# Performance work log

Measured on AMD Instinct MI355X. Metric: run time of the kernel, lower is better.

The kernel has to match this reference:

```python
import jax, jax.numpy as jnp
import numpy as np

B, L, D_IN, D_MODEL, D_STATE, D_DISCR, KER = 2, 1024, 512, 1024, 16, 64, 4


def setup_inputs() -> dict:
    ks = jax.random.split(jax.random.key(0), 9)
    s = 0.02
    return {
        "seq": jax.random.normal(ks[0], (B, L, D_IN), jnp.float32),
        "W_in": jax.random.normal(ks[1], (2 * D_MODEL, D_IN), jnp.float32) * s,
        "W_out": jax.random.normal(ks[2], (D_IN, D_MODEL), jnp.float32) * s,
        "W_B": jax.random.normal(ks[3], (D_STATE, D_MODEL), jnp.float32) * s,
        "W_C": jax.random.normal(ks[4], (D_STATE, D_MODEL), jnp.float32) * s,
        "W_D1": jax.random.normal(ks[5], (D_DISCR, D_MODEL), jnp.float32) * s,
        "W_D2": jax.random.normal(ks[6], (D_MODEL, D_DISCR), jnp.float32) * s,
        "conv_w": jax.random.normal(ks[7], (D_MODEL, 1, KER), jnp.float32) * 0.1,
        "conv_b": jax.random.normal(ks[8], (D_MODEL,), jnp.float32) * 0.01,
        "A": jnp.tile(jnp.arange(1, D_STATE + 1, dtype=jnp.float32), (D_MODEL, 1)),
        "D": jnp.ones((D_MODEL,), jnp.float32),
    }


def _causal_depthwise_conv(x, w, b):
    # x: [B, L, D] -> torch Conv1d(groups=D, padding=KER-1) truncated to first L outputs
    x = jnp.swapaxes(x, 1, 2)  # [B, D, L]
    y = jax.lax.conv_general_dilated(
        x, w, window_strides=(1,), padding=[(KER - 1, 0)],
        dimension_numbers=("NCH", "OIH", "NCH"), feature_group_count=D_MODEL)
    y = y + b[None, :, None]
    return jnp.swapaxes(y, 1, 2)  # [B, L, D]


def _ssm(x, W_B, W_C, W_D1, W_D2, A, D):
    # x: [B, L, D]
    exp_negA = jnp.exp(-A)                                  # [D, S]
    Bm = jnp.einsum("bld,sd->bls", x, W_B)                  # [B, L, S]
    Cm = jnp.einsum("bld,sd->bls", x, W_C)                  # [B, L, S]
    delta = jax.nn.softplus(D + jnp.einsum("ble,de->bld", jnp.einsum("bld,ed->ble", x, W_D1), W_D2))  # [B, L, D]
    A_bar = exp_negA[None, None] * delta[..., None]         # [B, L, D, S]
    X = Bm[:, :, None, :] * delta[..., None] * x[..., None]  # [B, L, D, S]

    def comb(c1, c2):
        a1, x1 = c1
        a2, x2 = c2
        return a1 * a2, a2 * x1 + x2

    _, h = jax.lax.associative_scan(comb, (A_bar, X), axis=1)  # h: [B, L, D, S]
    y = jnp.einsum("blds,bls->bld", h, Cm)
    return y + D * x


def reference(seq, W_in, W_out, W_B, W_C, W_D1, W_D2, conv_w, conv_b, A, D):
    ab = jnp.einsum("bli,oi->blo", seq, W_in)   # [B, L, 2*D_MODEL]
    a, b = ab[..., :D_MODEL], ab[..., D_MODEL:]
    a = jax.nn.silu(_causal_depthwise_conv(a, conv_w, conv_b))
    a = _ssm(a, W_B, W_C, W_D1, W_D2, A, D)
    out = a * jax.nn.silu(b)
    return jnp.einsum("bld,od->blo", out, W_out)  # [B, L, D_IN]
```

## Files before the change

kernel.cpp:

```cpp
#include <hip/hip_runtime.h>
#include <hip/hip_bf16.h>

using bf16 = __hip_bfloat16;
typedef short short8 __attribute__((ext_vector_type(8)));
typedef float float4v __attribute__((ext_vector_type(4)));

#define B_   2
#define L_   1024
#define DIN  512
#define DM   1024
#define DS   16
#define DD   64
#define KER_ 4
#define NROW (B_*L_)

#define SD   8
#define SC   32
#define SLC  32
#define SDP  9

__device__ __forceinline__ float silu_f(float v){ return v / (1.f + expf(-v)); }

__device__ __forceinline__ short2 f2bf2(float a, float b) {
  __hip_bfloat162 h = __float22bfloat162_rn(float2{a, b});
  union { __hip_bfloat162 h; short2 s; } u; u.h = h; return u.s;
}

template<int MW, int NW, int MT, int NT, int EP, int KS, int B3SRC, int CONVA>
__global__ __launch_bounds__(256)
void mfma_nt(const float* __restrict__ A, const float* __restrict__ B,
             const float* __restrict__ B2, const float* __restrict__ B3,
             float* __restrict__ C, const float* __restrict__ Dv,
             const float* __restrict__ abp, const float* __restrict__ cw,
             const float* __restrict__ cb,
             int M, int N, int K, int lda, int ldb, int ldc) {
  constexpr int BM = MW * MT * 16;
  constexpr int BN = NW * NT * 16;
  constexpr int TU = (BM + BN) * 4;
  constexpr int NU = (TU + 255) / 256;
  __shared__ short As[BM * 40];
  __shared__ short Bs[BN * 40];
  const int m0 = blockIdx.y * BM;
  const int n0 = blockIdx.x * BN;
  const int tid  = threadIdx.x;
  const int lane = tid & 63;
  const int wave = tid >> 6;
  const int wm   = wave % MW;
  const int wn   = wave / MW;
  const int r16  = lane & 15;
  const int quad = lane >> 4;
  const int kb   = (KS > 1) ? blockIdx.z : 0;
  const int kper = K / KS;
  const int kbeg = kb * kper;
  const int kend = kbeg + kper;

  float4v acc[MT][NT];
#pragma unroll
  for (int i = 0; i < MT; i++)
#pragma unroll
    for (int j = 0; j < NT; j++) acc[i][j] = (float4v){0.f, 0.f, 0.f, 0.f};

  float4 pf0[NU], pf1[NU];
  auto ldu = [&](int j, int k0) {
    int u = tid + j * 256;
    if (u >= TU) return;
    if (CONVA && u < BM * 4) {
      int row = u >> 2, q = u & 3;
      int n = m0 + row, l = n & (L_ - 1), bq = n >> 10;
      float4 tap0[KER_], tap1[KER_];
#pragma unroll
      for (int t = 0; t < KER_; t++) {
        int ll = l - (KER_ - 1) + t;
        if (ll >= 0) {
          const float4* p = (const float4*)(abp + (size_t)(bq * L_ + ll) * lda + k0 + q * 8);
          tap0[t] = p[0]; tap1[t] = p[1];
        } else {
          tap0[t] = float4{0.f,0.f,0.f,0.f}; tap1[t] = float4{0.f,0.f,0.f,0.f};
        }
      }
      float r[8];
#pragma unroll
      for (int e = 0; e < 8; e++) {
        int d = k0 + q * 8 + e;
        float4 w = *(const float4*)(cw + d * 4);
        float a = cb[d];
#pragma unroll
        for (int t = 0; t < KER_; t++) {
          float te = (e < 4) ? (&tap0[t].x)[e] : (&tap1[t].x)[e - 4];
          a += te * (&w.x)[t];
        }
        r[e] = silu_f(a);
      }
      pf0[j] = float4{r[0], r[1], r[2], r[3]};
      pf1[j] = float4{r[4], r[5], r[6], r[7]};
      return;
    }
    const float4* p;
    if (u < BM * 4) {
      int row = u >> 2, q = u & 3;
      p = (const float4*)(A + (size_t)(m0 + row) * lda + k0 + q * 8);
    } else {
      int v = u - BM * 4; int row = v >> 2, q = v & 3;
      if (B3SRC) {
        int rr = n0 + row;
        const float* bp = (rr < 16) ? (B + (size_t)rr * ldb)
                        : (rr < 32) ? (B2 + (size_t)(rr - 16) * ldb)
                                    : (B3 + (size_t)(rr - 32) * ldb);
        p = (const float4*)(bp + k0 + q * 8);
      } else {
        p = (const float4*)(B + (size_t)(n0 + row) * ldb + k0 + q * 8);
      }
    }
    pf0[j] = p[0]; pf1[j] = p[1];
  };
  auto stu = [&](int j) {
    int u = tid + j * 256;
    if (u >= TU) return;
    short2 s0 = f2bf2(pf0[j].x, pf0[j].y), s1 = f2bf2(pf0[j].z, pf0[j].w);
    short2 s2 = f2bf2(pf1[j].x, pf1[j].y), s3 = f2bf2(pf1[j].z, pf1[j].w);
    short8 s = { s0.x, s0.y, s1.x, s1.y, s2.x, s2.y, s3.x, s3.y };
    if (u < BM * 4) {
      int row = u >> 2, q = u & 3;
      *(short8*)&As[row * 40 + q * 8] = s;
    } else {
      int v = u - BM * 4; int row = v >> 2, q = v & 3;
      *(short8*)&Bs[row * 40 + q * 8] = s;
    }
  };

#pragma unroll
  for (int j = 0; j < NU; j++) ldu(j, kbeg);

  for (int k0 = kbeg; k0 < kend; k0 += 32) {
#pragma unroll
    for (int j = 0; j < NU; j++) stu(j);
    __syncthreads();
    if (k0 + 32 < kend) {
#pragma unroll
      for (int j = 0; j < NU; j++) ldu(j, k0 + 32);
    }
    short8 afr[MT], bfr[NT];
#pragma unroll
    for (int mi = 0; mi < MT; mi++)
      afr[mi] = *(const short8*)&As[(wm * MT * 16 + mi * 16 + r16) * 40 + quad * 8];
#pragma unroll
    for (int ni = 0; ni < NT; ni++)
      bfr[ni] = *(const short8*)&Bs[(wn * NT * 16 + ni * 16 + r16) * 40 + quad * 8];
#pragma unroll
    for (int mi = 0; mi < MT; mi++)
#pragma unroll
      for (int ni = 0; ni < NT; ni++)
        acc[mi][ni] = __builtin_amdgcn_mfma_f32_16x16x32_bf16(
            afr[mi], bfr[ni], acc[mi][ni], 0, 0, 0);
    __syncthreads();
  }

  float* Cp = C + ((EP == 2) ? (size_t)0 : (size_t)kb * M * ldc);
#pragma unroll
  for (int mi = 0; mi < MT; mi++)
#pragma unroll
    for (int ni = 0; ni < NT; ni++) {
      int gn = n0 + wn * NT * 16 + ni * 16 + r16;
#pragma unroll
      for (int r = 0; r < 4; r++) {
        int gm = m0 + wm * MT * 16 + mi * 16 + quad * 4 + r;
        float v = acc[mi][ni][r];
        if (EP == 1) {
          v += Dv[gn];
          v = fmaxf(v, 0.f) + log1pf(expf(-fabsf(v)));
          Cp[(size_t)gm * ldc + gn] = v;
        } else if (EP == 2) {
          atomicAdd(&Cp[(size_t)gm * ldc + gn], v);
        } else {
          Cp[(size_t)gm * ldc + gn] = v;
        }
      }
    }
}

__global__ __launch_bounds__(256)
void scan_fused_k(const float* __restrict__ ab, const float* __restrict__ dlt,
                  const float* __restrict__ pall, const float* __restrict__ A,
                  const float* __restrict__ Dv, const float* __restrict__ cw,
                  const float* __restrict__ cb, float* __restrict__ sout) {
  __shared__ float Pl[SC][DS][SDP];
  __shared__ float Hl[SC][DS][SDP];
  const int blk = blockIdx.x;
  const int b   = blk >> 7;
  const int d0  = (blk & 127) * SD;
  const int dd  = threadIdx.x & (SD - 1);
  const int c   = threadIdx.x >> 3;
  const int d   = d0 + dd;

  float e[DS];
#pragma unroll
  for (int s = 0; s < DS; s++) e[s] = expf(-A[d * DS + s]);
  const int   lbase = c * SLC;
  const int   nbase = b * L_ + lbase;
  const float4 w    = *(const float4*)(cw + d * 4);
  const float  cbv  = cb[d];

  auto abA = [&](int l) -> float {
    return (l >= 0) ? ab[(size_t)(b * L_ + l) * (2 * DM) + d] : 0.f;
  };

  float r0 = abA(lbase - 3), r1 = abA(lbase - 2), r2 = abA(lbase - 1);
  float h[DS], p[DS];
#pragma unroll
  for (int s = 0; s < DS; s++) { h[s] = 0.f; p[s] = 1.f; }
  for (int i = 0; i < SLC; i++) {
    int n = nbase + i;
    float a3 = ab[(size_t)n * (2 * DM) + d];
    float xv = silu_f(cbv + r0 * w.x + r1 * w.y + r2 * w.z + a3 * w.w);
    r0 = r1; r1 = r2; r2 = a3;
    float dl = dlt[(size_t)n * DM + d];
    float dx = dl * xv;
    const float4* bm4 = (const float4*)(pall + (size_t)n * 96);
    float4 b0 = bm4[0], b1 = bm4[1], b2 = bm4[2], b3 = bm4[3];
    float bmv[DS] = { b0.x,b0.y,b0.z,b0.w, b1.x,b1.y,b1.z,b1.w,
                      b2.x,b2.y,b2.z,b2.w, b3.x,b3.y,b3.z,b3.w };
#pragma unroll
    for (int s = 0; s < DS; s++) {
      float a_ = e[s] * dl;
      h[s] = a_ * h[s] + bmv[s] * dx;
      p[s] *= a_;
    }
  }
#pragma unroll
  for (int s = 0; s < DS; s++) { Pl[c][s][dd] = p[s]; Hl[c][s][dd] = h[s]; }
  __syncthreads();

  if (threadIdx.x < DS * SD) {
    int s2  = threadIdx.x >> 3;
    int dd2 = threadIdx.x & (SD - 1);
    float H = 0.f;
    for (int c2 = 0; c2 < SC; c2++) {
      float pp = Pl[c2][s2][dd2];
      float hh = Hl[c2][s2][dd2];
      Pl[c2][s2][dd2] = H;
      H = pp * H + hh;
    }
  }
  __syncthreads();

#pragma unroll
  for (int s = 0; s < DS; s++) h[s] = Pl[c][s][dd];
  float Dd = Dv[d];
  r0 = abA(lbase - 3); r1 = abA(lbase - 2); r2 = abA(lbase - 1);
  for (int i = 0; i < SLC; i++) {
    int n = nbase + i;
    float a3 = ab[(size_t)n * (2 * DM) + d];
    float xv = silu_f(cbv + r0 * w.x + r1 * w.y + r2 * w.z + a3 * w.w);
    r0 = r1; r1 = r2; r2 = a3;
    float dl = dlt[(size_t)n * DM + d];
    float dx = dl * xv;
    const float4* bm4 = (const float4*)(pall + (size_t)n * 96);
    float4 b0 = bm4[0], b1 = bm4[1], b2 = bm4[2], b3 = bm4[3];
    float4 c0 = bm4[4], c1 = bm4[5], c2v = bm4[6], c3 = bm4[7];
    float bmv[DS] = { b0.x,b0.y,b0.z,b0.w, b1.x,b1.y,b1.z,b1.w,
                      b2.x,b2.y,b2.z,b2.w, b3.x,b3.y,b3.z,b3.w };
    float cmv[DS] = { c0.x,c0.y,c0.z,c0.w, c1.x,c1.y,c1.z,c1.w,
                      c2v.x,c2v.y,c2v.z,c2v.w, c3.x,c3.y,c3.z,c3.w };
    float y = 0.f;
#pragma unroll
    for (int s = 0; s < DS; s++) {
      h[s] = e[s] * dl * h[s] + bmv[s] * dx;
      y += h[s] * cmv[s];
    }
    y += Dd * xv;
    float g = ab[(size_t)n * (2 * DM) + DM + d];
    sout[(size_t)n * DM + d] = y * silu_f(g);
  }
}

extern "C" void kernel_launch(void* const* d_in, const int* in_sizes, int n_in,
                              void* d_out, int out_size, void* d_ws, size_t ws_size,
                              hipStream_t stream) {
  const float* seq  = (const float*)d_in[0];
  const float* Win  = (const float*)d_in[1];
  const float* Wout = (const float*)d_in[2];
  const float* WB   = (const float*)d_in[3];
  const float* WC   = (const float*)d_in[4];
  const float* WD1  = (const float*)d_in[5];
  const float* WD2  = (const float*)d_in[6];
  const float* cw   = (const float*)d_in[7];
  const float* cb   = (const float*)d_in[8];
  const float* A    = (const float*)d_in[9];
  const float* Dv   = (const float*)d_in[10];
  float* out = (float*)d_out;

  float* ws   = (float*)d_ws;
  float* ab   = ws;
  float* dlt  = ab   + 4194304;
  float* pall = dlt  + 2097152;
  float* sout = pall + 196608;
  float* t1   = pall + 32;

  hipMemsetAsync(out, 0, (size_t)NROW * DIN * 4, stream);
  hipMemsetAsync(pall, 0, (size_t)NROW * 96 * 4, stream);
  mfma_nt<2, 2, 4, 2, 0, 1, 0, 0><<<dim3((2 * DM) / 64, NROW / 128, 1), 256, 0, stream>>>(
      seq, Win, nullptr, nullptr, ab, nullptr, nullptr, nullptr, nullptr,
      NROW, 2 * DM, DIN, DIN, DIN, 2 * DM);
  mfma_nt<4, 1, 1, 6, 2, 8, 1, 1><<<dim3(1, NROW / 64, 8), 256, 0, stream>>>(
      nullptr, WB, WC, WD1, pall, nullptr, ab, cw, cb,
      NROW, 96, DM, 2 * DM, DM, 96);
  mfma_nt<2, 2, 2, 2, 1, 1, 0, 0><<<dim3(DM / 64, NROW / 64, 1), 256, 0, stream>>>(
      t1, WD2, nullptr, nullptr, dlt, Dv, nullptr, nullptr, nullptr,
      NROW, DM, DD, 96, DD, DM);
  scan_fused_k<<<B_ * (DM / SD), 256, 0, stream>>>(ab, dlt, pall, A, Dv, cw, cb, sout);
  mfma_nt<2, 2, 2, 2, 2, 2, 0, 0><<<dim3(DIN / 64, NROW / 64, 2), 256, 0, stream>>>(
      sout, Wout, nullptr, nullptr, out, nullptr, nullptr, nullptr, nullptr,
      NROW, DIN, DM, DM, DM, DIN);
}
```

Baseline: 180.4 us.

## Fuse all stages into one persistent kernel with grid barriers

Replaces five kernel launches and two memsets with a single persistent 256-block kernel that runs the input GEMM, the B/C/delta projection, the chunked scan and the output GEMM as phases separated by atomic grid barriers. The delta projection is fused into the projection phase through a shared-memory t1 tile, and split-K atomics are dropped so the memsets go away. The aim is to cut launch gaps and memset overhead, at the cost of fixed tiling per phase, idle blocks in the projection phase (only 128 of 256 work), half the threads idle during the scan, and a reliance on all 256 blocks being co-resident for the barriers.

```diff
diff --git a/kernel.cpp b/kernel.cpp
--- a/kernel.cpp
+++ b/kernel.cpp
@@ -1,7 +1,6 @@
 #include <hip/hip_runtime.h>
 #include <hip/hip_bf16.h>
 
-using bf16 = __hip_bfloat16;
 typedef short short8 __attribute__((ext_vector_type(8)));
 typedef float float4v __attribute__((ext_vector_type(4)));
 
@@ -13,6 +12,8 @@
 #define DD   64
 #define KER_ 4
 #define NROW (B_*L_)
+#define NBLK 256
+#define NTHR 512
 
 #define SD   8
 #define SC   32
@@ -25,251 +26,322 @@
   __hip_bfloat162 h = __float22bfloat162_rn(float2{a, b});
   union { __hip_bfloat162 h; short2 s; } u; u.h = h; return u.s;
 }
-
-template<int MW, int NW, int MT, int NT, int EP, int KS, int B3SRC, int CONVA>
-__global__ __launch_bounds__(256)
-void mfma_nt(const float* __restrict__ A, const float* __restrict__ B,
-             const float* __restrict__ B2, const float* __restrict__ B3,
-             float* __restrict__ C, const float* __restrict__ Dv,
-             const float* __restrict__ abp, const float* __restrict__ cw,
-             const float* __restrict__ cb,
-             int M, int N, int K, int lda, int ldb, int ldc) {
-  constexpr int BM = MW * MT * 16;
-  constexpr int BN = NW * NT * 16;
-  constexpr int TU = (BM + BN) * 4;
-  constexpr int NU = (TU + 255) / 256;
-  __shared__ short As[BM * 40];
-  __shared__ short Bs[BN * 40];
-  const int m0 = blockIdx.y * BM;
-  const int n0 = blockIdx.x * BN;
+__device__ __forceinline__ short f2bf1(float a) {
+  __hip_bfloat16 h = __float2bfloat16(a);
+  union { __hip_bfloat16 h; short s; } u; u.h = h; return u.s;
+}
+__device__ __forceinline__ short8 pack8(const float4& x0, const float4& x1) {
+  short2 s0 = f2bf2(x0.x, x0.y), s1 = f2bf2(x0.z, x0.w);
+  short2 s2 = f2bf2(x1.x, x1.y), s3 = f2bf2(x1.z, x1.w);
+  return short8{ s0.x, s0.y, s1.x, s1.y, s2.x, s2.y, s3.x, s3.y };
+}
+
+union SMem {
+  struct { short As[128 * 40]; short Bs[128 * 40]; } g1;
+  struct { short xs[16 * 40]; short wsb[96 * 40]; short t1s[16 * 72]; } pj;
+  struct { float Pl[SC][DS][SDP]; float Hl[SC][DS][SDP]; } sc;
+  struct { short As[64 * 40]; short Bs[64 * 40]; } g2;
+};
+
+__device__ __forceinline__ void grid_barrier(unsigned* cnt, unsigned nblk) {
+  __syncthreads();
+  if (threadIdx.x == 0) {
+    __threadfence();
+    __hip_atomic_fetch_add(cnt, 1u, __ATOMIC_ACQ_REL, __HIP_MEMORY_SCOPE_AGENT);
+    while (__hip_atomic_load(cnt, __ATOMIC_ACQUIRE, __HIP_MEMORY_SCOPE_AGENT) < nblk)
+      __builtin_amdgcn_s_sleep(1);
+  }
+  __syncthreads();
+  __threadfence();
+}
+
+__global__ __launch_bounds__(NTHR)
+void mega_k(const float* __restrict__ seq, const float* __restrict__ Win,
+            const float* __restrict__ Wout, const float* __restrict__ WB,
+            const float* __restrict__ WC, const float* __restrict__ WD1,
+            const float* __restrict__ WD2, const float* __restrict__ cw,
+            const float* __restrict__ cb, const float* __restrict__ Aa,
+            const float* __restrict__ Dv, float* __restrict__ out,
+            float* __restrict__ ab, float* __restrict__ dlt,
+            float* __restrict__ pall, float* __restrict__ sout,
+            unsigned* __restrict__ bar) {
+  __shared__ SMem sm;
+  const int blk  = blockIdx.x;
   const int tid  = threadIdx.x;
   const int lane = tid & 63;
   const int wave = tid >> 6;
-  const int wm   = wave % MW;
-  const int wn   = wave / MW;
   const int r16  = lane & 15;
   const int quad = lane >> 4;
-  const int kb   = (KS > 1) ? blockIdx.z : 0;
-  const int kper = K / KS;
-  const int kbeg = kb * kper;
-  const int kend = kbeg + kper;
-
-  float4v acc[MT][NT];
-#pragma unroll
-  for (int i = 0; i < MT; i++)
-#pragma unroll
-    for (int j = 0; j < NT; j++) acc[i][j] = (float4v){0.f, 0.f, 0.f, 0.f};
-
-  float4 pf0[NU], pf1[NU];
-  auto ldu = [&](int j, int k0) {
-    int u = tid + j * 256;
-    if (u >= TU) return;
-    if (CONVA && u < BM * 4) {
-      int row = u >> 2, q = u & 3;
-      int n = m0 + row, l = n & (L_ - 1), bq = n >> 10;
-      float4 tap0[KER_], tap1[KER_];
-#pragma unroll
-      for (int t = 0; t < KER_; t++) {
-        int ll = l - (KER_ - 1) + t;
-        if (ll >= 0) {
-          const float4* p = (const float4*)(abp + (size_t)(bq * L_ + ll) * lda + k0 + q * 8);
-          tap0[t] = p[0]; tap1[t] = p[1];
-        } else {
-          tap0[t] = float4{0.f,0.f,0.f,0.f}; tap1[t] = float4{0.f,0.f,0.f,0.f};
+
+  {
+    const int m0 = (blk >> 4) * 128;
+    const int n0 = (blk & 15) * 128;
+    const int wm = wave & 1, wn = wave >> 1;
+    float4v acc[4][2];
+#pragma unroll
+    for (int i = 0; i < 4; i++)
+#pragma unroll
+      for (int j = 0; j < 2; j++) acc[i][j] = (float4v){0.f, 0.f, 0.f, 0.f};
+    float4 pf0[2], pf1[2];
+    auto ldu = [&](int j, int k0) {
+      int u = tid + j * 512;
+      const float4* p;
+      if (u < 512) { int row = u >> 2, q = u & 3;
+        p = (const float4*)(seq + (size_t)(m0 + row) * DIN + k0 + q * 8);
+      } else { int v = u - 512; int row = v >> 2, q = v & 3;
+        p = (const float4*)(Win + (size_t)(n0 + row) * DIN + k0 + q * 8);
+      }
+      pf0[j] = p[0]; pf1[j] = p[1];
+    };
+    auto stu = [&](int j) {
+      int u = tid + j * 512;
+      short8 s = pack8(pf0[j], pf1[j]);
+      if (u < 512) { int row = u >> 2, q = u & 3; *(short8*)&sm.g1.As[row * 40 + q * 8] = s; }
+      else { int v = u - 512; int row = v >> 2, q = v & 3; *(short8*)&sm.g1.Bs[row * 40 + q * 8] = s; }
+    };
+    ldu(0, 0); ldu(1, 0);
+    for (int k0 = 0; k0 < DIN; k0 += 32) {
+      stu(0); stu(1);
+      __syncthreads();
+      if (k0 + 32 < DIN) { ldu(0, k0 + 32); ldu(1, k0 + 32); }
+      short8 afr[4], bfr[2];
+#pragma unroll
+      for (int mi = 0; mi < 4; mi++)
+        afr[mi] = *(const short8*)&sm.g1.As[(wm * 64 + mi * 16 + r16) * 40 + quad * 8];
+#pragma unroll
+      for (int ni = 0; ni < 2; ni++)
+        bfr[ni] = *(const short8*)&sm.g1.Bs[(wn * 32 + ni * 16 + r16) * 40 + quad * 8];
+#pragma unroll
+      for (int mi = 0; mi < 4; mi++)
+#pragma unroll
+        for (int ni = 0; ni < 2; ni++)
+          acc[mi][ni] = __builtin_amdgcn_mfma_f32_16x16x32_bf16(afr[mi], bfr[ni], acc[mi][ni], 0, 0, 0);
+      __syncthreads();
+    }
+#pragma unroll
+    for (int mi = 0; mi < 4; mi++)
+#pragma unroll
+      for (int ni = 0; ni < 2; ni++)
+#pragma unroll
+        for (int r = 0; r < 4; r++)
+          ab[(size_t)(m0 + wm * 64 + mi * 16 + quad * 4 + r) * (2 * DM)
+             + n0 + wn * 32 + ni * 16 + r16] = acc[mi][ni][r];
+  }
+  grid_barrier(bar + 0, NBLK);
+
+  if (blk < 128) {
+    const int m0 = blk * 16;
+    const int bq = m0 >> 10;
+    float4v accp = (float4v){0.f, 0.f, 0.f, 0.f};
+    for (int k0 = 0; k0 < DM; k0 += 32) {
+      if (tid < 64) {
+        int row = tid >> 2, q = tid & 3;
+        int n = m0 + row, l = n & (L_ - 1);
+        float4 tap0[KER_], tap1[KER_];
+#pragma unroll
+        for (int t = 0; t < KER_; t++) {
+          int ll = l - (KER_ - 1) + t;
+          if (ll >= 0) {
+            const float4* p = (const float4*)(ab + (size_t)(bq * L_ + ll) * (2 * DM) + k0 + q * 8);
+            tap0[t] = p[0]; tap1[t] = p[1];
+          } else { tap0[t] = float4{0.f,0.f,0.f,0.f}; tap1[t] = float4{0.f,0.f,0.f,0.f}; }
         }
-      }
-      float r[8];
-#pragma unroll
-      for (int e = 0; e < 8; e++) {
-        int d = k0 + q * 8 + e;
-        float4 w = *(const float4*)(cw + d * 4);
-        float a = cb[d];
-#pragma unroll
-        for (int t = 0; t < KER_; t++) {
-          float te = (e < 4) ? (&tap0[t].x)[e] : (&tap1[t].x)[e - 4];
-          a += te * (&w.x)[t];
+        float r8[8];
+#pragma unroll
+        for (int e = 0; e < 8; e++) {
+          int d = k0 + q * 8 + e;
+          float4 w = *(const float4*)(cw + d * 4);
+          float a = cb[d];
+#pragma unroll
+          for (int t = 0; t < KER_; t++) {
+            float te = (e < 4) ? (&tap0[t].x)[e] : (&tap1[t].x)[e - 4];
+            a += te * (&w.x)[t];
+          }
+          r8[e] = silu_f(a);
         }
-        r[e] = silu_f(a);
-      }
-      pf0[j] = float4{r[0], r[1], r[2], r[3]};
-      pf1[j] = float4{r[4], r[5], r[6], r[7]};
-      return;
-    }
-    const float4* p;
-    if (u < BM * 4) {
-      int row = u >> 2, q = u & 3;
-      p = (const float4*)(A + (size_t)(m0 + row) * lda + k0 + q * 8);
-    } else {
-      int v = u - BM * 4; int row = v >> 2, q = v & 3;
-      if (B3SRC) {
-        int rr = n0 + row;
-        const float* bp = (rr < 16) ? (B + (size_t)rr * ldb)
-                        : (rr < 32) ? (B2 + (size_t)(rr - 16) * ldb)
-                                    : (B3 + (size_t)(rr - 32) * ldb);
-        p = (const float4*)(bp + k0 + q * 8);
-      } else {
-        p = (const float4*)(B + (size_t)(n0 + row) * ldb + k0 + q * 8);
-      }
-    }
-    pf0[j] = p[0]; pf1[j] = p[1];
-  };
-  auto stu = [&](int j) {
-    int u = tid + j * 256;
-    if (u >= TU) return;
-    short2 s0 = f2bf2(pf0[j].x, pf0[j].y), s1 = f2bf2(pf0[j].z, pf0[j].w);
-    short2 s2 = f2bf2(pf1[j].x, pf1[j].y), s3 = f2bf2(pf1[j].z, pf1[j].w);
-    short8 s = { s0.x, s0.y, s1.x, s1.y, s2.x, s2.y, s3.x, s3.y };
-    if (u < BM * 4) {
-      int row = u >> 2, q = u & 3;
-      *(short8*)&As[row * 40 + q * 8] = s;
-    } else {
-      int v = u - BM * 4; int row = v >> 2, q = v & 3;
-      *(short8*)&Bs[row * 40 + q * 8] = s;
-    }
-  };
-
-#pragma unroll
-  for (int j = 0; j < NU; j++) ldu(j, kbeg);
-
-  for (int k0 = kbeg; k0 < kend; k0 += 32) {
-#pragma unroll
-    for (int j = 0; j < NU; j++) stu(j);
+        *(short8*)&sm.pj.xs[row * 40 + q * 8] =
+            pack8(float4{r8[0], r8[1], r8[2], r8[3]}, float4{r8[4], r8[5], r8[6], r8[7]});
+      } else if (tid < 448) {
+        int t2 = tid - 64, row = t2 >> 2, q = t2 & 3;
+        const float* bp = (row < 16) ? (WB + (size_t)row * DM)
+                        : (row < 32) ? (WC + (size_t)(row - 16) * DM)
+                                     : (WD1 + (size_t)(row - 32) * DM);
+        const float4* p = (const float4*)(bp + k0 + q * 8);
+        *(short8*)&sm.pj.wsb[row * 40 + q * 8] = pack8(p[0], p[1]);
+      }
+      __syncthreads();
+      if (wave < 6) {
+        short8 afr = *(const short8*)&sm.pj.xs[r16 * 40 + quad * 8];
+        short8 bfr = *(const short8*)&sm.pj.wsb[(wave * 16 + r16) * 40 + quad * 8];
+        accp = __builtin_amdgcn_mfma_f32_16x16x32_bf16(afr, bfr, accp, 0, 0, 0);
+      }
+      __syncthreads();
+    }
+    if (wave < 6) {
+      int gl = wave * 16 + r16;
+#pragma unroll
+      for (int r = 0; r < 4; r++) {
+        int lr = quad * 4 + r;
+        float v = accp[r];
+        if (gl < 32) pall[(size_t)(m0 + lr) * 96 + gl] = v;
+        else         sm.pj.t1s[lr * 72 + (gl - 32)] = f2bf1(v);
+      }
+    }
     __syncthreads();
-    if (k0 + 32 < kend) {
-#pragma unroll
-      for (int j = 0; j < NU; j++) ldu(j, k0 + 32);
-    }
-    short8 afr[MT], bfr[NT];
-#pragma unroll
-    for (int mi = 0; mi < MT; mi++)
-      afr[mi] = *(const short8*)&As[(wm * MT * 16 + mi * 16 + r16) * 40 + quad * 8];
-#pragma unroll
-    for (int ni = 0; ni < NT; ni++)
-      bfr[ni] = *(const short8*)&Bs[(wn * NT * 16 + ni * 16 + r16) * 40 + quad * 8];
-#pragma unroll
-    for (int mi = 0; mi < MT; mi++)
-#pragma unroll
-      for (int ni = 0; ni < NT; ni++)
-        acc[mi][ni] = __builtin_amdgcn_mfma_f32_16x16x32_bf16(
-            afr[mi], bfr[ni], acc[mi][ni], 0, 0, 0);
+    for (int cb2 = 0; cb2 < 8; cb2++) {
+      int n0d = wave * 128 + cb2 * 16;
+      float4v accd = (float4v){0.f, 0.f, 0.f, 0.f};
+#pragma unroll
+      for (int ks = 0; ks < DD; ks += 32) {
+        short8 afr = *(const short8*)&sm.pj.t1s[r16 * 72 + ks + quad * 8];
+        const float4* p = (const float4*)(WD2 + (size_t)(n0d + r16) * DD + ks + quad * 8);
+        short8 bfr = pack8(p[0], p[1]);
+        accd = __builtin_amdgcn_mfma_f32_16x16x32_bf16(afr, bfr, accd, 0, 0, 0);
+      }
+      int gn = n0d + r16;
+      float dvn = Dv[gn];
+#pragma unroll
+      for (int r = 0; r < 4; r++) {
+        float v = accd[r] + dvn;
+        v = fmaxf(v, 0.f) + log1pf(expf(-fabsf(v)));
+        dlt[(size_t)(m0 + quad * 4 + r) * DM + gn] = v;
+      }
+    }
+  }
+  grid_barrier(bar + 1, NBLK);
+
+  {
+    const int b   = blk >> 7;
+    const int d0  = (blk & 127) * SD;
+    const bool act = tid < 256;
+    const int dd  = tid & (SD - 1);
+    const int c   = (tid >> 3) & 31;
+    const int d   = d0 + dd;
+    float e[DS], h[DS], p[DS];
+    float4 w = {0.f,0.f,0.f,0.f};
+    float cbv = 0.f, Dd = 0.f;
+    const int lbase = c * SLC;
+    const int nbase = b * L_ + lbase;
+    if (act) {
+#pragma unroll
+      for (int s = 0; s < DS; s++) e[s] = expf(-Aa[d * DS + s]);
+      w = *(const float4*)(cw + d * 4);
+      cbv = cb[d];
+      Dd  = Dv[d];
+    }
+    auto abA = [&](int l) -> float {
+      return (l >= 0) ? ab[(size_t)(b * L_ + l) * (2 * DM) + d] : 0.f;
+    };
+    if (act) {
+      float r0 = abA(lbase - 3), r1 = abA(lbase - 2), r2 = abA(lbase - 1);
+#pragma unroll
+      for (int s = 0; s < DS; s++) { h[s] = 0.f; p[s] = 1.f; }
+      for (int i = 0; i < SLC; i++) {
+        int n = nbase + i;
+        float a3 = ab[(size_t)n * (2 * DM) + d];
+        float xv = silu_f(cbv + r0 * w.x + r1 * w.y + r2 * w.z + a3 * w.w);
+        r0 = r1; r1 = r2; r2 = a3;
+        float dl = dlt[(size_t)n * DM + d];
+        float dx = dl * xv;
+        const float4* bm4 = (const float4*)(pall + (size_t)n * 96);
+        float4 b0 = bm4[0], b1 = bm4[1], b2 = bm4[2], b3 = bm4[3];
+        float bmv[DS] = { b0.x,b0.y,b0.z,b0.w, b1.x,b1.y,b1.z,b1.w,
+                          b2.x,b2.y,b2.z,b2.w, b3.x,b3.y,b3.z,b3.w };
+#pragma unroll
+        for (int s = 0; s < DS; s++) {
+          float a_ = e[s] * dl;
+          h[s] = a_ * h[s] + bmv[s] * dx;
+          p[s] *= a_;
+        }
+      }
+#pragma unroll
+      for (int s = 0; s < DS; s++) { sm.sc.Pl[c][s][dd] = p[s]; sm.sc.Hl[c][s][dd] = h[s]; }
+    }
     __syncthreads();
-  }
-
-  float* Cp = C + ((EP == 2) ? (size_t)0 : (size_t)kb * M * ldc);
-#pragma unroll
-  for (int mi = 0; mi < MT; mi++)
-#pragma unroll
-    for (int ni = 0; ni < NT; ni++) {
-      int gn = n0 + wn * NT * 16 + ni * 16 + r16;
-#pragma unroll
-      for (int r = 0; r < 4; r++) {
-        int gm = m0 + wm * MT * 16 + mi * 16 + quad * 4 + r;
-        float v = acc[mi][ni][r];
-        if (EP == 1) {
-          v += Dv[gn];
-          v = fmaxf(v, 0.f) + log1pf(expf(-fabsf(v)));
-          Cp[(size_t)gm * ldc + gn] = v;
-        } else if (EP == 2) {
-          atomicAdd(&Cp[(size_t)gm * ldc + gn], v);
-        } else {
-          Cp[(size_t)gm * ldc + gn] = v;
+    if (tid < DS * SD) {
+      int s2  = tid >> 3;
+      int dd2 = tid & (SD - 1);
+      float H = 0.f;
+      for (int c2 = 0; c2 < SC; c2++) {
+        float pp = sm.sc.Pl[c2][s2][dd2];
+        float hh = sm.sc.Hl[c2][s2][dd2];
+        sm.sc.Pl[c2][s2][dd2] = H;
+        H = pp * H + hh;
+      }
+    }
+    __syncthreads();
+    if (act) {
+#pragma unroll
+      for (int s = 0; s < DS; s++) h[s] = sm.sc.Pl[c][s][dd];
+      float r0 = abA(lbase - 3), r1 = abA(lbase - 2), r2 = abA(lbase - 1);
+      for (int i = 0; i < SLC; i++) {
+        int n = nbase + i;
+        float a3 = ab[(size_t)n * (2 * DM) + d];
+        float xv = silu_f(cbv + r0 * w.x + r1 * w.y + r2 * w.z + a3 * w.w);
+        r0 = r1; r1 = r2; r2 = a3;
+        float dl = dlt[(size_t)n * DM + d];
+        float dx = dl * xv;
+        const float4* bm4 = (const float4*)(pall + (size_t)n * 96);
+        float4 b0 = bm4[0], b1 = bm4[1], b2 = bm4[2], b3 = bm4[3];
+        float4 c0 = bm4[4], c1 = bm4[5], c2v = bm4[6], c3 = bm4[7];
+        float bmv[DS] = { b0.x,b0.y,b0.z,b0.w, b1.x,b1.y,b1.z,b1.w,
+                          b2.x,b2.y,b2.z,b2.w, b3.x,b3.y,b3.z,b3.w };
+        float cmv[DS] = { c0.x,c0.y,c0.z,c0.w, c1.x,c1.y,c1.z,c1.w,
+                          c2v.x,c2v.y,c2v.z,c2v.w, c3.x,c3.y,c3.z,c3.w };
+        float y = 0.f;
+#pragma unroll
+        for (int s = 0; s < DS; s++) {
+          h[s] = e[s] * dl * h[s] + bmv[s] * dx;
+          y += h[s] * cmv[s];
         }
-      }
-    }
-}
-
-__global__ __launch_bounds__(256)
-void scan_fused_k(const float* __restrict__ ab, const float* __restrict__ dlt,
-                  const float* __restrict__ pall, const float* __restrict__ A,
-                  const float* __restrict__ Dv, const float* __restrict__ cw,
-                  const float* __restrict__ cb, float* __restrict__ sout) {
-  __shared__ float Pl[SC][DS][SDP];
-  __shared__ float Hl[SC][DS][SDP];
-  const int blk = blockIdx.x;
-  const int b   = blk >> 7;
-  const int d0  = (blk & 127) * SD;
-  const int dd  = threadIdx.x & (SD - 1);
-  const int c   = threadIdx.x >> 3;
-  const int d   = d0 + dd;
-
-  float e[DS];
-#pragma unroll
-  for (int s = 0; s < DS; s++) e[s] = expf(-A[d * DS + s]);
-  const int   lbase = c * SLC;
-  const int   nbase = b * L_ + lbase;
-  const float4 w    = *(const float4*)(cw + d * 4);
-  const float  cbv  = cb[d];
-
-  auto abA = [&](int l) -> float {
-    return (l >= 0) ? ab[(size_t)(b * L_ + l) * (2 * DM) + d] : 0.f;
-  };
-
-  float r0 = abA(lbase - 3), r1 = abA(lbase - 2), r2 = abA(lbase - 1);
-  float h[DS], p[DS];
-#pragma unroll
-  for (int s = 0; s < DS; s++) { h[s] = 0.f; p[s] = 1.f; }
-  for (int i = 0; i < SLC; i++) {
-    int n = nbase + i;
-    float a3 = ab[(size_t)n * (2 * DM) + d];
-    float xv = silu_f(cbv + r0 * w.x + r1 * w.y + r2 * w.z + a3 * w.w);
-    r0 = r1; r1 = r2; r2 = a3;
-    float dl = dlt[(size_t)n * DM + d];
-    float dx = dl * xv;
-    const float4* bm4 = (const float4*)(pall + (size_t)n * 96);
-    float4 b0 = bm4[0], b1 = bm4[1], b2 = bm4[2], b3 = bm4[3];
-    float bmv[DS] = { b0.x,b0.y,b0.z,b0.w, b1.x,b1.y,b1.z,b1.w,
-                      b2.x,b2.y,b2.z,b2.w, b3.x,b3.y,b3.z,b3.w };
-#pragma unroll
-    for (int s = 0; s < DS; s++) {
-      float a_ = e[s] * dl;
-      h[s] = a_ * h[s] + bmv[s] * dx;
-      p[s] *= a_;
-    }
-  }
-#pragma unroll
-  for (int s = 0; s < DS; s++) { Pl[c][s][dd] = p[s]; Hl[c][s][dd] = h[s]; }
-  __syncthreads();
-
-  if (threadIdx.x < DS * SD) {
-    int s2  = threadIdx.x >> 3;
-    int dd2 = threadIdx.x & (SD - 1);
-    float H = 0.f;
-    for (int c2 = 0; c2 < SC; c2++) {
-      float pp = Pl[c2][s2][dd2];
-      float hh = Hl[c2][s2][dd2];
-      Pl[c2][s2][dd2] = H;
-      H = pp * H + hh;
-    }
-  }
-  __syncthreads();
-
-#pragma unroll
-  for (int s = 0; s < DS; s++) h[s] = Pl[c][s][dd];
-  float Dd = Dv[d];
-  r0 = abA(lbase - 3); r1 = abA(lbase - 2); r2 = abA(lbase - 1);
-  for (int i = 0; i < SLC; i++) {
-    int n = nbase + i;
-    float a3 = ab[(size_t)n * (2 * DM) + d];
-    float xv = silu_f(cbv + r0 * w.x + r1 * w.y + r2 * w.z + a3 * w.w);
-    r0 = r1; r1 = r2; r2 = a3;
-    float dl = dlt[(size_t)n * DM + d];
-    float dx = dl * xv;
-    const float4* bm4 = (const float4*)(pall + (size_t)n * 96);
-    float4 b0 = bm4[0], b1 = bm4[1], b2 = bm4[2], b3 = bm4[3];
-    float4 c0 = bm4[4], c1 = bm4[5], c2v = bm4[6], c3 = bm4[7];
-    float bmv[DS] = { b0.x,b0.y,b0.z,b0.w, b1.x,b1.y,b1.z,b1.w,
-                      b2.x,b2.y,b2.z,b2.w, b3.x,b3.y,b3.z,b3.w };
-    float cmv[DS] = { c0.x,c0.y,c0.z,c0.w, c1.x,c1.y,c1.z,c1.w,
-                      c2v.x,c2v.y,c2v.z,c2v.w, c3.x,c3.y,c3.z,c3.w };
-    float y = 0.f;
-#pragma unroll
-    for (int s = 0; s < DS; s++) {
-      h[s] = e[s] * dl * h[s] + bmv[s] * dx;
-      y += h[s] * cmv[s];
-    }
-    y += Dd * xv;
-    float g = ab[(size_t)n * (2 * DM) + DM + d];
-    sout[(size_t)n * DM + d] = y * silu_f(g);
+        y += Dd * xv;
+        float g = ab[(size_t)n * (2 * DM) + DM + d];
+        sout[(size_t)n * DM + d] = y * silu_f(g);
+      }
+    }
+  }
+  grid_barrier(bar + 2, NBLK);
+
+  {
+    const int m0 = (blk >> 3) * 64;
+    const int n0 = (blk & 7) * 64;
+    const int wm = wave & 1, wn = wave >> 1;
+    float4v acc[2];
+    acc[0] = (float4v){0.f, 0.f, 0.f, 0.f};
+    acc[1] = (float4v){0.f, 0.f, 0.f, 0.f};
+    float4 pf0, pf1;
+    auto ldu = [&](int k0) {
+      const float4* p;
+      if (tid < 256) { int row = tid >> 2, q = tid & 3;
+        p = (const float4*)(sout + (size_t)(m0 + row) * DM + k0 + q * 8);
+      } else { int v = tid - 256; int row = v >> 2, q = v & 3;
+        p = (const float4*)(Wout + (size_t)(n0 + row) * DM + k0 + q * 8);
+      }
+      pf0 = p[0]; pf1 = p[1];
+    };
+    auto stu = [&]() {
+      short8 s = pack8(pf0, pf1);
+      if (tid < 256) { int row = tid >> 2, q = tid & 3; *(short8*)&sm.g2.As[row * 40 + q * 8] = s; }
+      else { int v = tid - 256; int row = v >> 2, q = v & 3; *(short8*)&sm.g2.Bs[row * 40 + q * 8] = s; }
+    };
+    ldu(0);
+    for (int k0 = 0; k0 < DM; k0 += 32) {
+      stu();
+      __syncthreads();
+      if (k0 + 32 < DM) ldu(k0 + 32);
+      short8 afr[2], bfr;
+      afr[0] = *(const short8*)&sm.g2.As[(wm * 32 + r16) * 40 + quad * 8];
+      afr[1] = *(const short8*)&sm.g2.As[(wm * 32 + 16 + r16) * 40 + quad * 8];
+      bfr    = *(const short8*)&sm.g2.Bs[(wn * 16 + r16) * 40 + quad * 8];
+      acc[0] = __builtin_amdgcn_mfma_f32_16x16x32_bf16(afr[0], bfr, acc[0], 0, 0, 0);
+      acc[1] = __builtin_amdgcn_mfma_f32_16x16x32_bf16(afr[1], bfr, acc[1], 0, 0, 0);
+      __syncthreads();
+    }
+#pragma unroll
+    for (int mi = 0; mi < 2; mi++)
+#pragma unroll
+      for (int r = 0; r < 4; r++)
+        out[(size_t)(m0 + wm * 32 + mi * 16 + quad * 4 + r) * DIN + n0 + wn * 16 + r16] = acc[mi][r];
   }
 }
 
@@ -294,21 +366,9 @@
   float* dlt  = ab   + 4194304;
   float* pall = dlt  + 2097152;
   float* sout = pall + 196608;
-  float* t1   = pall + 32;
-
-  hipMemsetAsync(out, 0, (size_t)NROW * DIN * 4, stream);
-  hipMemsetAsync(pall, 0, (size_t)NROW * 96 * 4, stream);
-  mfma_nt<2, 2, 4, 2, 0, 1, 0, 0><<<dim3((2 * DM) / 64, NROW / 128, 1), 256, 0, stream>>>(
-      seq, Win, nullptr, nullptr, ab, nullptr, nullptr, nullptr, nullptr,
-      NROW, 2 * DM, DIN, DIN, DIN, 2 * DM);
-  mfma_nt<4, 1, 1, 6, 2, 8, 1, 1><<<dim3(1, NROW / 64, 8), 256, 0, stream>>>(
-      nullptr, WB, WC, WD1, pall, nullptr, ab, cw, cb,
-      NROW, 96, DM, 2 * DM, DM, 96);
-  mfma_nt<2, 2, 2, 2, 1, 1, 0, 0><<<dim3(DM / 64, NROW / 64, 1), 256, 0, stream>>>(
-      t1, WD2, nullptr, nullptr, dlt, Dv, nullptr, nullptr, nullptr,
-      NROW, DM, DD, 96, DD, DM);
-  scan_fused_k<<<B_ * (DM / SD), 256, 0, stream>>>(ab, dlt, pall, A, Dv, cw, cb, sout);
-  mfma_nt<2, 2, 2, 2, 2, 2, 0, 0><<<dim3(DIN / 64, NROW / 64, 2), 256, 0, stream>>>(
-      sout, Wout, nullptr, nullptr, out, nullptr, nullptr, nullptr, nullptr,
-      NROW, DIN, DM, DM, DM, DIN);
-}
+  unsigned* bar = (unsigned*)(sout + 2097152);
+
+  hipMemsetAsync(bar, 0, 64, stream);
+  mega_k<<<NBLK, NTHR, 0, stream>>>(seq, Win, Wout, WB, WC, WD1, WD2, cw, cb,
+                                    A, Dv, out, ab, dlt, pall, sout, bar);
+}
```

Result: slower. 470.6 us (+160.8%).
